# Performance work log

Measured on AMD Instinct MI355X. Metric: run time of the kernel, lower is better.

## Reference

```python
import jax, jax.numpy as jnp
import numpy as np

NEG_SLOPE = 0.2
LN_EPS = 1e-5


def setup_inputs() -> dict:
    key = jax.random.key(0)
    kx, kw, ks, kd = jax.random.split(key, 4)
    B, T, C, Fin, Fout = 32, 256, 64, 128, 128
    x = jax.random.normal(kx, (B, T, C, Fin), dtype=jnp.float32)
    W = jax.random.normal(kw, (Fin, Fout), dtype=jnp.float32) * (1.0 / np.sqrt(Fin))
    attn_src = jax.random.normal(ks, (Fout,), dtype=jnp.float32) * 0.1
    attn_dst = jax.random.normal(kd, (Fout,), dtype=jnp.float32) * 0.1
    gamma = jnp.ones((Fout,), dtype=jnp.float32)
    beta = jnp.zeros((Fout,), dtype=jnp.float32)
    return {"x": x, "W": W, "attn_src": attn_src, "attn_dst": attn_dst,
            "gamma": gamma, "beta": beta}


def reference(x, W, attn_src, attn_dst, gamma, beta):
    # h: (B,T,C,Fout)
    h = jnp.einsum('btci,io->btco', x, W)
    src = jnp.einsum('btcf,f->btc', h, attn_src)  # score of node as source
    dst = jnp.einsum('btcf,f->btc', h, attn_dst)  # score of node as dest
    # e[b,t,i,j] = src[b,t,i] + dst[b,t,j]
    e = src[..., :, None] + dst[..., None, :]
    e = jnp.where(e >= 0, e, NEG_SLOPE * e)  # leaky_relu
    alpha = jax.nn.softmax(e, axis=-1)       # softmax over neighbors j
    out = jnp.einsum('btij,btjf->btif', alpha, h)
    # LayerNorm over feature dim
    mu = jnp.mean(out, axis=-1, keepdims=True)
    var = jnp.var(out, axis=-1, keepdims=True)
    out = (out - mu) * jax.lax.rsqrt(var + LN_EPS) * gamma + beta
    return jax.nn.relu(out)
```

## Files before the change

### kernel.cpp

```cpp
#include <hip/hip_runtime.h>


typedef __attribute__((ext_vector_type(8))) short short8;
typedef __attribute__((ext_vector_type(4))) float f32x4;

constexpr int   NTILES    = 8192;
constexpr int   GRID      = 512;
constexpr float NEG_SLOPE = 0.2f;
constexpr float LN_EPS    = 1e-5f;

__device__ __forceinline__ unsigned short f2bf(float f) {
    unsigned int u = __builtin_bit_cast(unsigned int, f);
    return (unsigned short)((u + 0x7FFFu + ((u >> 16) & 1u)) >> 16);
}
__device__ __forceinline__ unsigned swz256(int row, int bytecol) {
    return (unsigned)(row * 256 + bytecol) ^ (unsigned)((row & 7) << 4);
}
__device__ __forceinline__ unsigned swz128(int row, int bytecol) {
    return (unsigned)(row * 128 + bytecol) ^ (unsigned)((row & 7) << 4);
}

#define LBAR() do { asm volatile("s_waitcnt lgkmcnt(0)"); __builtin_amdgcn_s_barrier(); } while (0)

__launch_bounds__(256, 2)
__global__ void gat_mfma6(const float* __restrict__ x,
                          const float* __restrict__ W,
                          const float* __restrict__ a_src,
                          const float* __restrict__ a_dst,
                          const float* __restrict__ gamma,
                          const float* __restrict__ beta,
                          float* __restrict__ out)
{
    __shared__ __align__(16) unsigned short sWt[128 * 128];
    __shared__ __align__(16) unsigned short sX [64 * 128];
    __shared__ __align__(16) unsigned short sHt[128 * 64];
    __shared__ __align__(16) float s_src[64];
    __shared__ __align__(16) float s_dst[64];
    __shared__ __align__(16) float s_g[128];
    __shared__ __align__(16) float s_b[128];

    unsigned short* sP   = sX;
    float*          s_ws = (float*)sHt;
    float*          s_wd = (float*)sHt + 128;

    const int t    = threadIdx.x;
    const int lane = t & 63;
    const int w    = t >> 6;
    const int l15  = lane & 15;
    const int lg   = lane >> 4;

    if (t < 128) {
        const float4* W4  = reinterpret_cast<const float4*>(W) + t * 32;
        const float4* as4 = reinterpret_cast<const float4*>(a_src);
        const float4* ad4 = reinterpret_cast<const float4*>(a_dst);
        float ws = 0.f, wd = 0.f;
        for (int n4 = 0; n4 < 32; ++n4) {
            float4 wr = W4[n4], as = as4[n4], ad = ad4[n4];
            ws += wr.x*as.x + wr.y*as.y + wr.z*as.z + wr.w*as.w;
            wd += wr.x*ad.x + wr.y*ad.y + wr.z*ad.z + wr.w*ad.w;
        }
        s_ws[t] = ws; s_wd[t] = wd;
        s_g[t] = gamma[t]; s_b[t] = beta[t];
    }

    {
        const float4* W4 = reinterpret_cast<const float4*>(W);
        for (int c = 0; c < 16; ++c) {
            int idx4 = t + 256 * c;
            float4 v = W4[idx4];
            int k  = idx4 >> 5;
            int n0 = (idx4 & 31) << 2;
            *(unsigned short*)((char*)sWt + swz256(n0 + 0, k * 2)) = f2bf(v.x);
            *(unsigned short*)((char*)sWt + swz256(n0 + 1, k * 2)) = f2bf(v.y);
            *(unsigned short*)((char*)sWt + swz256(n0 + 2, k * 2)) = f2bf(v.z);
            *(unsigned short*)((char*)sWt + swz256(n0 + 3, k * 2)) = f2bf(v.w);
        }
    }
    __syncthreads();

    float wsr[8], wdr[8];
    {
        const int k0 = (t & 15) * 8;
        #pragma unroll
        for (int q = 0; q < 8; ++q) { wsr[q] = s_ws[k0 + q]; wdr[q] = s_wd[k0 + q]; }
    }

    float4 px[8];
    {
        const float4* x4 = reinterpret_cast<const float4*>(x + (size_t)blockIdx.x * 8192);
        #pragma unroll
        for (int c = 0; c < 4; ++c) {
            const int idx8 = t + 256 * c;
            px[2*c]   = x4[idx8 * 2];
            px[2*c+1] = x4[idx8 * 2 + 1];
        }
    }

    for (int tile = blockIdx.x; tile < NTILES; tile += GRID) {
        float* ob = out + (size_t)tile * 8192;

        #pragma unroll
        for (int c = 0; c < 4; ++c) {
            const float4 v0 = px[2*c], v1 = px[2*c+1];
            float ps = v0.x*wsr[0] + v0.y*wsr[1] + v0.z*wsr[2] + v0.w*wsr[3]
                     + v1.x*wsr[4] + v1.y*wsr[5] + v1.z*wsr[6] + v1.w*wsr[7];
            float pd = v0.x*wdr[0] + v0.y*wdr[1] + v0.z*wdr[2] + v0.w*wdr[3]
                     + v1.x*wdr[4] + v1.y*wdr[5] + v1.z*wdr[6] + v1.w*wdr[7];
            uint4 pk;
            pk.x = (unsigned)f2bf(v0.x) | ((unsigned)f2bf(v0.y) << 16);
            pk.y = (unsigned)f2bf(v0.z) | ((unsigned)f2bf(v0.w) << 16);
            pk.z = (unsigned)f2bf(v1.x) | ((unsigned)f2bf(v1.y) << 16);
            pk.w = (unsigned)f2bf(v1.z) | ((unsigned)f2bf(v1.w) << 16);
            const int m = (t >> 4) + 16 * c;
            *(uint4*)((char*)sX + swz256(m, (t & 15) * 16)) = pk;
            #pragma unroll
            for (int msk = 1; msk < 16; msk <<= 1) {
                ps += __shfl_xor(ps, msk, 64);
                pd += __shfl_xor(pd, msk, 64);
            }
            if ((t & 15) == 0) { s_src[m] = ps; s_dst[m] = pd; }
        }

        if (tile + GRID < NTILES) {
            const float4* xn = reinterpret_cast<const float4*>(x + (size_t)(tile + GRID) * 8192);
            #pragma unroll
            for (int c = 0; c < 4; ++c) {
                const int idx8 = t + 256 * c;
                px[2*c]   = xn[idx8 * 2];
                px[2*c+1] = xn[idx8 * 2 + 1];
            }
        }
        LBAR();

        f32x4 acc[4][2];
        #pragma unroll
        for (int mi = 0; mi < 4; ++mi) {
            acc[mi][0] = f32x4{0.f,0.f,0.f,0.f};
            acc[mi][1] = f32x4{0.f,0.f,0.f,0.f};
        }
        #pragma unroll
        for (int kb = 0; kb < 4; ++kb) {
            const int kbyte = kb * 64 + lg * 16;
            short8 bfr0 = *(const short8*)((char*)sWt + swz256(32 * w +  0 + l15, kbyte));
            short8 bfr1 = *(const short8*)((char*)sWt + swz256(32 * w + 16 + l15, kbyte));
            #pragma unroll
            for (int mi = 0; mi < 4; ++mi) {
                short8 afr = *(const short8*)((char*)sX + swz256(mi * 16 + l15, kbyte));
                acc[mi][0] = __builtin_amdgcn_mfma_f32_16x16x32_bf16(afr, bfr0, acc[mi][0], 0, 0, 0);
                acc[mi][1] = __builtin_amdgcn_mfma_f32_16x16x32_bf16(afr, bfr1, acc[mi][1], 0, 0, 0);
            }
        }
        #pragma unroll
        for (int mi = 0; mi < 4; ++mi) {
            const int m0 = mi * 16 + lg * 4;
            #pragma unroll
            for (int nb = 0; nb < 2; ++nb) {
                const int n = 32 * w + nb * 16 + l15;
                uint2 pk;
                pk.x = (unsigned)f2bf(acc[mi][nb][0]) | ((unsigned)f2bf(acc[mi][nb][1]) << 16);
                pk.y = (unsigned)f2bf(acc[mi][nb][2]) | ((unsigned)f2bf(acc[mi][nb][3]) << 16);
                *(uint2*)((char*)sHt + swz128(n, m0 * 2)) = pk;
            }
        }
        LBAR();

        {
            const int i = t >> 2, jg = t & 3;
            const float srci = s_src[i];
            float e[16];
            float mx = -1e30f;
            #pragma unroll
            for (int q = 0; q < 16; ++q) {
                float v = srci + s_dst[jg * 16 + q];
                v = (v >= 0.f) ? v : NEG_SLOPE * v;
                e[q] = v;
                mx = fmaxf(mx, v);
            }
            mx = fmaxf(mx, __shfl_xor(mx, 1, 64));
            mx = fmaxf(mx, __shfl_xor(mx, 2, 64));
            float sm = 0.f;
            #pragma unroll
            for (int q = 0; q < 16; ++q) { e[q] = __expf(e[q] - mx); sm += e[q]; }
            sm += __shfl_xor(sm, 1, 64);
            sm += __shfl_xor(sm, 2, 64);
            const float inv = 1.0f / sm;
            unsigned short a_[16];
            #pragma unroll
            for (int q = 0; q < 16; ++q) a_[q] = f2bf(e[q] * inv);
            uint4 pk0, pk1;
            pk0.x = (unsigned)a_[0]  | ((unsigned)a_[1]  << 16);
            pk0.y = (unsigned)a_[2]  | ((unsigned)a_[3]  << 16);
            pk0.z = (unsigned)a_[4]  | ((unsigned)a_[5]  << 16);
            pk0.w = (unsigned)a_[6]  | ((unsigned)a_[7]  << 16);
            pk1.x = (unsigned)a_[8]  | ((unsigned)a_[9]  << 16);
            pk1.y = (unsigned)a_[10] | ((unsigned)a_[11] << 16);
            pk1.z = (unsigned)a_[12] | ((unsigned)a_[13] << 16);
            pk1.w = (unsigned)a_[14] | ((unsigned)a_[15] << 16);
            *(uint4*)((char*)sP + swz128(i, jg * 32))      = pk0;
            *(uint4*)((char*)sP + swz128(i, jg * 32 + 16)) = pk1;
        }
        LBAR();

        f32x4 o[8];
        #pragma unroll
        for (int mi = 0; mi < 8; ++mi) o[mi] = f32x4{0.f,0.f,0.f,0.f};
        #pragma unroll
        for (int kb = 0; kb < 2; ++kb) {
            const int jbyte = kb * 64 + lg * 16;
            short8 bfr = *(const short8*)((char*)sP + swz128(w * 16 + l15, jbyte));
            #pragma unroll
            for (int mi = 0; mi < 8; ++mi) {
                short8 afr = *(const short8*)((char*)sHt + swz128(mi * 16 + l15, jbyte));
                o[mi] = __builtin_amdgcn_mfma_f32_16x16x32_bf16(afr, bfr, o[mi], 0, 0, 0);
            }
        }

        float sm1 = 0.f, sm2 = 0.f;
        #pragma unroll
        for (int mi = 0; mi < 8; ++mi) {
            #pragma unroll
            for (int r = 0; r < 4; ++r) { const float v = o[mi][r]; sm1 += v; sm2 += v * v; }
        }
        sm1 += __shfl_xor(sm1, 16, 64); sm2 += __shfl_xor(sm2, 16, 64);
        sm1 += __shfl_xor(sm1, 32, 64); sm2 += __shfl_xor(sm2, 32, 64);
        const float mu   = sm1 * (1.f / 128.f);
        const float var  = sm2 * (1.f / 128.f) - mu * mu;
        const float rstd = rsqrtf(var + LN_EPS);

        float* orow = ob + (w * 16 + l15) * 128;
        #pragma unroll
        for (int mi = 0; mi < 8; ++mi) {
            const int n0 = mi * 16 + lg * 4;
            const float4 gv = *(const float4*)&s_g[n0];
            const float4 bv = *(const float4*)&s_b[n0];
            float4 vo;
            vo.x = fmaxf((o[mi][0] - mu) * rstd * gv.x + bv.x, 0.f);
            vo.y = fmaxf((o[mi][1] - mu) * rstd * gv.y + bv.y, 0.f);
            vo.z = fmaxf((o[mi][2] - mu) * rstd * gv.z + bv.z, 0.f);
            vo.w = fmaxf((o[mi][3] - mu) * rstd * gv.w + bv.w, 0.f);
            *(float4*)(orow + n0) = vo;
        }
        LBAR();
    }
}

extern "C" void kernel_launch(void* const* d_in, const int* in_sizes, int n_in,
                              void* d_out, int out_size, void* d_ws, size_t ws_size,
                              hipStream_t stream) {
    const float* x   = (const float*)d_in[0];
    const float* W   = (const float*)d_in[1];
    const float* asv = (const float*)d_in[2];
    const float* adv = (const float*)d_in[3];
    const float* gm  = (const float*)d_in[4];
    const float* bt  = (const float*)d_in[5];
    float* out = (float*)d_out;

    hipLaunchKernelGGL(gat_mfma6, dim3(GRID), dim3(256), 0, stream,
                       x, W, asv, adv, gm, bt, out);
}
```

Measured before the change: 122.4 us.

## Keep attention probabilities in registers, alias H onto X buffer, raise occupancy

```diff
diff --git a/kernel.cpp b/kernel.cpp
--- a/kernel.cpp
+++ b/kernel.cpp
@@ -5,7 +5,7 @@
 typedef __attribute__((ext_vector_type(4))) float f32x4;
 
 constexpr int   NTILES    = 8192;
-constexpr int   GRID      = 512;
+constexpr int   GRID      = 768;
 constexpr float NEG_SLOPE = 0.2f;
 constexpr float LN_EPS    = 1e-5f;
 
@@ -13,6 +13,9 @@
     unsigned int u = __builtin_bit_cast(unsigned int, f);
     return (unsigned short)((u + 0x7FFFu + ((u >> 16) & 1u)) >> 16);
 }
+__device__ __forceinline__ unsigned pack2(float lo, float hi) {
+    return (unsigned)f2bf(lo) | ((unsigned)f2bf(hi) << 16);
+}
 __device__ __forceinline__ unsigned swz256(int row, int bytecol) {
     return (unsigned)(row * 256 + bytecol) ^ (unsigned)((row & 7) << 4);
 }
@@ -22,8 +25,8 @@
 
 #define LBAR() do { asm volatile("s_waitcnt lgkmcnt(0)"); __builtin_amdgcn_s_barrier(); } while (0)
 
-__launch_bounds__(256, 2)
-__global__ void gat_mfma6(const float* __restrict__ x,
+__launch_bounds__(256, 3)
+__global__ void gat_mfma7(const float* __restrict__ x,
                           const float* __restrict__ W,
                           const float* __restrict__ a_src,
                           const float* __restrict__ a_dst,
@@ -32,16 +35,13 @@
                           float* __restrict__ out)
 {
     __shared__ __align__(16) unsigned short sWt[128 * 128];
-    __shared__ __align__(16) unsigned short sX [64 * 128];
-    __shared__ __align__(16) unsigned short sHt[128 * 64];
+    __shared__ __align__(16) unsigned short sXH[64 * 128];
     __shared__ __align__(16) float s_src[64];
     __shared__ __align__(16) float s_dst[64];
+    __shared__ __align__(16) float s_ws[128];
+    __shared__ __align__(16) float s_wd[128];
     __shared__ __align__(16) float s_g[128];
     __shared__ __align__(16) float s_b[128];
-
-    unsigned short* sP   = sX;
-    float*          s_ws = (float*)sHt;
-    float*          s_wd = (float*)sHt + 128;
 
     const int t    = threadIdx.x;
     const int lane = t & 63;
@@ -107,12 +107,10 @@
             float pd = v0.x*wdr[0] + v0.y*wdr[1] + v0.z*wdr[2] + v0.w*wdr[3]
                      + v1.x*wdr[4] + v1.y*wdr[5] + v1.z*wdr[6] + v1.w*wdr[7];
             uint4 pk;
-            pk.x = (unsigned)f2bf(v0.x) | ((unsigned)f2bf(v0.y) << 16);
-            pk.y = (unsigned)f2bf(v0.z) | ((unsigned)f2bf(v0.w) << 16);
-            pk.z = (unsigned)f2bf(v1.x) | ((unsigned)f2bf(v1.y) << 16);
-            pk.w = (unsigned)f2bf(v1.z) | ((unsigned)f2bf(v1.w) << 16);
+            pk.x = pack2(v0.x, v0.y); pk.y = pack2(v0.z, v0.w);
+            pk.z = pack2(v1.x, v1.y); pk.w = pack2(v1.z, v1.w);
             const int m = (t >> 4) + 16 * c;
-            *(uint4*)((char*)sX + swz256(m, (t & 15) * 16)) = pk;
+            *(uint4*)((char*)sXH + swz256(m, (t & 15) * 16)) = pk;
             #pragma unroll
             for (int msk = 1; msk < 16; msk <<= 1) {
                 ps += __shfl_xor(ps, msk, 64);
@@ -145,11 +143,47 @@
             short8 bfr1 = *(const short8*)((char*)sWt + swz256(32 * w + 16 + l15, kbyte));
             #pragma unroll
             for (int mi = 0; mi < 4; ++mi) {
-                short8 afr = *(const short8*)((char*)sX + swz256(mi * 16 + l15, kbyte));
+                short8 afr = *(const short8*)((char*)sXH + swz256(mi * 16 + l15, kbyte));
                 acc[mi][0] = __builtin_amdgcn_mfma_f32_16x16x32_bf16(afr, bfr0, acc[mi][0], 0, 0, 0);
                 acc[mi][1] = __builtin_amdgcn_mfma_f32_16x16x32_bf16(afr, bfr1, acc[mi][1], 0, 0, 0);
             }
         }
+
+        short8 pa0, pa1;
+        {
+            const float srci = s_src[w * 16 + l15];
+            const float4 dA0 = *(const float4*)&s_dst[lg * 8];
+            const float4 dA1 = *(const float4*)&s_dst[lg * 8 + 4];
+            const float4 dB0 = *(const float4*)&s_dst[32 + lg * 8];
+            const float4 dB1 = *(const float4*)&s_dst[32 + lg * 8 + 4];
+            float e[16] = { srci+dA0.x, srci+dA0.y, srci+dA0.z, srci+dA0.w,
+                            srci+dA1.x, srci+dA1.y, srci+dA1.z, srci+dA1.w,
+                            srci+dB0.x, srci+dB0.y, srci+dB0.z, srci+dB0.w,
+                            srci+dB1.x, srci+dB1.y, srci+dB1.z, srci+dB1.w };
+            float mx = -1e30f;
+            #pragma unroll
+            for (int q = 0; q < 16; ++q) {
+                e[q] = (e[q] >= 0.f) ? e[q] : NEG_SLOPE * e[q];
+                mx = fmaxf(mx, e[q]);
+            }
+            mx = fmaxf(mx, __shfl_xor(mx, 16, 64));
+            mx = fmaxf(mx, __shfl_xor(mx, 32, 64));
+            float sm = 0.f;
+            #pragma unroll
+            for (int q = 0; q < 16; ++q) { e[q] = __expf(e[q] - mx); sm += e[q]; }
+            sm += __shfl_xor(sm, 16, 64);
+            sm += __shfl_xor(sm, 32, 64);
+            const float inv = 1.0f / sm;
+            uint4 p0, p1;
+            p0.x = pack2(e[0]*inv,  e[1]*inv);  p0.y = pack2(e[2]*inv,  e[3]*inv);
+            p0.z = pack2(e[4]*inv,  e[5]*inv);  p0.w = pack2(e[6]*inv,  e[7]*inv);
+            p1.x = pack2(e[8]*inv,  e[9]*inv);  p1.y = pack2(e[10]*inv, e[11]*inv);
+            p1.z = pack2(e[12]*inv, e[13]*inv); p1.w = pack2(e[14]*inv, e[15]*inv);
+            pa0 = __builtin_bit_cast(short8, p0);
+            pa1 = __builtin_bit_cast(short8, p1);
+        }
+        LBAR();
+
         #pragma unroll
         for (int mi = 0; mi < 4; ++mi) {
             const int m0 = mi * 16 + lg * 4;
@@ -157,47 +191,10 @@
             for (int nb = 0; nb < 2; ++nb) {
                 const int n = 32 * w + nb * 16 + l15;
                 uint2 pk;
-                pk.x = (unsigned)f2bf(acc[mi][nb][0]) | ((unsigned)f2bf(acc[mi][nb][1]) << 16);
-                pk.y = (unsigned)f2bf(acc[mi][nb][2]) | ((unsigned)f2bf(acc[mi][nb][3]) << 16);
-                *(uint2*)((char*)sHt + swz128(n, m0 * 2)) = pk;
-            }
-        }
-        LBAR();
-
-        {
-            const int i = t >> 2, jg = t & 3;
-            const float srci = s_src[i];
-            float e[16];
-            float mx = -1e30f;
-            #pragma unroll
-            for (int q = 0; q < 16; ++q) {
-                float v = srci + s_dst[jg * 16 + q];
-                v = (v >= 0.f) ? v : NEG_SLOPE * v;
-                e[q] = v;
-                mx = fmaxf(mx, v);
-            }
-            mx = fmaxf(mx, __shfl_xor(mx, 1, 64));
-            mx = fmaxf(mx, __shfl_xor(mx, 2, 64));
-            float sm = 0.f;
-            #pragma unroll
-            for (int q = 0; q < 16; ++q) { e[q] = __expf(e[q] - mx); sm += e[q]; }
-            sm += __shfl_xor(sm, 1, 64);
-            sm += __shfl_xor(sm, 2, 64);
-            const float inv = 1.0f / sm;
-            unsigned short a_[16];
-            #pragma unroll
-            for (int q = 0; q < 16; ++q) a_[q] = f2bf(e[q] * inv);
-            uint4 pk0, pk1;
-            pk0.x = (unsigned)a_[0]  | ((unsigned)a_[1]  << 16);
-            pk0.y = (unsigned)a_[2]  | ((unsigned)a_[3]  << 16);
-            pk0.z = (unsigned)a_[4]  | ((unsigned)a_[5]  << 16);
-            pk0.w = (unsigned)a_[6]  | ((unsigned)a_[7]  << 16);
-            pk1.x = (unsigned)a_[8]  | ((unsigned)a_[9]  << 16);
-            pk1.y = (unsigned)a_[10] | ((unsigned)a_[11] << 16);
-            pk1.z = (unsigned)a_[12] | ((unsigned)a_[13] << 16);
-            pk1.w = (unsigned)a_[14] | ((unsigned)a_[15] << 16);
-            *(uint4*)((char*)sP + swz128(i, jg * 32))      = pk0;
-            *(uint4*)((char*)sP + swz128(i, jg * 32 + 16)) = pk1;
+                pk.x = pack2(acc[mi][nb][0], acc[mi][nb][1]);
+                pk.y = pack2(acc[mi][nb][2], acc[mi][nb][3]);
+                *(uint2*)((char*)sXH + swz128(n, m0 * 2)) = pk;
+            }
         }
         LBAR();
 
@@ -207,10 +204,10 @@
         #pragma unroll
         for (int kb = 0; kb < 2; ++kb) {
             const int jbyte = kb * 64 + lg * 16;
-            short8 bfr = *(const short8*)((char*)sP + swz128(w * 16 + l15, jbyte));
+            const short8 bfr = (kb == 0) ? pa0 : pa1;
             #pragma unroll
             for (int mi = 0; mi < 8; ++mi) {
-                short8 afr = *(const short8*)((char*)sHt + swz128(mi * 16 + l15, jbyte));
+                short8 afr = *(const short8*)((char*)sXH + swz128(mi * 16 + l15, jbyte));
                 o[mi] = __builtin_amdgcn_mfma_f32_16x16x32_bf16(afr, bfr, o[mi], 0, 0, 0);
             }
         }
@@ -255,6 +252,6 @@
     const float* bt  = (const float*)d_in[5];
     float* out = (float*)d_out;
 
-    hipLaunchKernelGGL(gat_mfma6, dim3(GRID), dim3(256), 0, stream,
+    hipLaunchKernelGGL(gat_mfma7, dim3(GRID), dim3(256), 0, stream,
                        x, W, asv, adv, gm, bt, out);
 }
```

Result: slower. 132.3 us (+8.1%).
